# Performance work log

Measured on AMD Instinct MI355X. Metric: run time of the kernel, lower is better.

Reference implementation:

```python
import jax, jax.numpy as jnp
import numpy as np

BN_EPS = 1e-5

def setup_inputs() -> dict:
    key = jax.random.key(0)
    ks = jax.random.split(key, 12)
    B = 32768
    x = jax.random.normal(ks[0], (B, 1, 28, 28), dtype=jnp.float32)
    conv_w = jax.random.normal(ks[1], (5, 1, 6, 6), dtype=jnp.float32) * 0.1
    conv_b = jax.random.normal(ks[2], (5,), dtype=jnp.float32) * 0.1
    bn2_gamma = jnp.ones((5,), jnp.float32) + jax.random.normal(ks[3], (5,), jnp.float32) * 0.05
    bn2_beta = jax.random.normal(ks[4], (5,), jnp.float32) * 0.05
    bn2_mean = jax.random.normal(ks[5], (5,), jnp.float32) * 0.1
    bn2_var = jax.random.uniform(ks[6], (5,), jnp.float32, 0.5, 1.5)
    fc_w = jax.random.normal(ks[7], (10, 125), dtype=jnp.float32) * 0.1
    fc_b = jax.random.normal(ks[8], (10,), dtype=jnp.float32) * 0.1
    bn1_gamma = jnp.ones((10,), jnp.float32) + jax.random.normal(ks[9], (10,), jnp.float32) * 0.05
    bn1_beta = jax.random.normal(ks[10], (10,), jnp.float32) * 0.05
    bn1_mean = jax.random.normal(ks[11], (10,), jnp.float32) * 0.1
    bn1_var = jnp.ones((10,), jnp.float32)
    return {"x": x, "conv_w": conv_w, "conv_b": conv_b,
            "bn2_gamma": bn2_gamma, "bn2_beta": bn2_beta, "bn2_mean": bn2_mean, "bn2_var": bn2_var,
            "fc_w": fc_w, "fc_b": fc_b,
            "bn1_gamma": bn1_gamma, "bn1_beta": bn1_beta, "bn1_mean": bn1_mean, "bn1_var": bn1_var}

def _sign(t):
    # torch Binarize = tensor.sign()
    return jnp.sign(t)

def reference(x, conv_w, conv_b, bn2_gamma, bn2_beta, bn2_mean, bn2_var,
              fc_w, fc_b, bn1_gamma, bn1_beta, bn1_mean, bn1_var):
    # BinarizeConv2d: binarize both input (C_in=1 != 3) and weight
    xb = _sign(x)
    wb = _sign(conv_w)
    y = jax.lax.conv_general_dilated(
        xb, wb, window_strides=(6, 6), padding=((2, 2), (2, 2)),
        dimension_numbers=("NCHW", "OIHW", "NCHW"))  # [B,5,5,5]
    y = y + conv_b[None, :, None, None]
    # BatchNorm2d (eval-mode running stats)
    y = (y - bn2_mean[None, :, None, None]) * (bn2_gamma / jnp.sqrt(bn2_var + BN_EPS))[None, :, None, None] + bn2_beta[None, :, None, None]
    # Hardtanh
    y = jnp.clip(y, -1.0, 1.0)
    # flatten to [B, 125]
    y = y.reshape(-1, 125)
    # BinarizeLinear: binarize input (125 != 784) and weight
    z = _sign(y) @ _sign(fc_w).T + fc_b
    # BatchNorm1d
    z = (z - bn1_mean) * (bn1_gamma / jnp.sqrt(bn1_var + BN_EPS)) + bn1_beta
    return jax.nn.log_softmax(z, axis=1)
```

## Files before the change

### kernel.cpp

```cpp
#include <hip/hip_runtime.h>
#include <cstdint>

#define BLK 256
#define WAVES 4
#define SPW 4
#define SPB (WAVES*SPW)
#define WPS 196
#define HDRW 16
#define SLAB (SPW*WPS)
#define XS_INTS (HDRW + WAVES*SLAB)
#define YS_W 33
#define YSLAB (SPW*YS_W)

#define W0_OFF  0
#define W1P_OFF 30
#define FC_OFF  45
#define CSC_OFF 375
#define CBI_OFF 380
#define FSC_OFF 385
#define FBI_OFF 395
#define WS_TOT  405

#if defined(__has_builtin)
# if __has_builtin(__builtin_amdgcn_sdot4)
#  define HAVE_SDOT4 1
# endif
#endif

__device__ __forceinline__ int dot4i8(int a, int b, int c) {
#ifdef HAVE_SDOT4
    return __builtin_amdgcn_sdot4(a, b, c, false);
#else
    int r = c;
    r += (((int)(a << 24)) >> 24) * (((int)(b << 24)) >> 24);
    r += (((int)(a << 16)) >> 24) * (((int)(b << 16)) >> 24);
    r += (((int)(a <<  8)) >> 24) * (((int)(b <<  8)) >> 24);
    r += (a >> 24) * (b >> 24);
    return r;
#endif
}

__device__ __forceinline__ int pack_sign4(float4 v) {
    int b0 = (v.x > 0.f) - (v.x < 0.f);
    int b1 = (v.y > 0.f) - (v.y < 0.f);
    int b2 = (v.z > 0.f) - (v.z < 0.f);
    int b3 = (v.w > 0.f) - (v.w < 0.f);
    return (b0 & 0xFF) | ((b1 & 0xFF) << 8) | ((b2 & 0xFF) << 16) | (b3 << 24);
}

__device__ __forceinline__ int sign8(float f) { return (f > 0.f) - (f < 0.f); }

__global__ __launch_bounds__(BLK, 4)
void bnn_fused(const float* __restrict__ x,
               const float* __restrict__ conv_w, const float* __restrict__ conv_b,
               const float* __restrict__ bn2_g,  const float* __restrict__ bn2_b,
               const float* __restrict__ bn2_m,  const float* __restrict__ bn2_v,
               const float* __restrict__ fc_w,   const float* __restrict__ fc_b,
               const float* __restrict__ bn1_g,  const float* __restrict__ bn1_b,
               const float* __restrict__ bn1_m,  const float* __restrict__ bn1_v,
               float* __restrict__ out)
{
    __shared__ int xsi[XS_INTS];
    __shared__ int ysi[WAVES * YSLAB];
    __shared__ int wsS[WS_TOT];

    const int tid  = threadIdx.x;
    const int lane = tid & 63;
    const int wid  = tid >> 6;
    const int blk  = blockIdx.x;

    const float4* xg = (const float4*)x + ((size_t)blk * SPB + wid * SPW) * WPS;
    float4 v[12]; float4 vr;
    #pragma unroll
    for (int k = 0; k < 12; k++) v[k] = xg[lane + k * 64];
    const bool hasr = lane < (SLAB - 12 * 64);
    if (hasr) vr = xg[lane + 12 * 64];

    if (tid < 30) {
        int c = tid / 6, kr = tid - c * 6;
        const float* wp = conv_w + c * 36 + kr * 6;
        uint32_t a = 0;
        #pragma unroll
        for (int k = 0; k < 4; k++) a |= (uint32_t)(sign8(wp[k]) & 0xFF) << (8 * k);
        wsS[W0_OFF + tid] = (int)a;
    } else if (tid >= 32 && tid < 47) {
        int i = tid - 32, c = i / 3, p = i - c * 3;
        const float* wp = conv_w + c * 36;
        uint32_t a = 0;
        a |= (uint32_t)(sign8(wp[(2*p)*6 + 4]) & 0xFF);
        a |= (uint32_t)(sign8(wp[(2*p)*6 + 5]) & 0xFF) << 8;
        a |= (uint32_t)(sign8(wp[(2*p+1)*6 + 4]) & 0xFF) << 16;
        a |= (uint32_t)(sign8(wp[(2*p+1)*6 + 5]) & 0xFF) << 24;
        wsS[W1P_OFF + i] = (int)a;
    } else if (tid >= 48 && tid < 53) {
        int c = tid - 48;
        float sc = bn2_g[c] / sqrtf(bn2_v[c] + 1e-5f);
        wsS[CSC_OFF + c] = __float_as_int(sc);
        wsS[CBI_OFF + c] = __float_as_int((conv_b[c] - bn2_m[c]) * sc + bn2_b[c]);
    } else if (tid >= 64 && tid < 74) {
        int o = tid - 64;
        float sc = bn1_g[o] / sqrtf(bn1_v[o] + 1e-5f);
        wsS[FSC_OFF + o] = __float_as_int(sc);
        wsS[FBI_OFF + o] = __float_as_int((fc_b[o] - bn1_m[o]) * sc + bn1_b[o]);
    }
    for (int i = tid; i < 330; i += BLK) {
        int o = i / 33, w = i - o * 33;
        uint32_t m = 0;
        #pragma unroll
        for (int k = 0; k < 4; k++) {
            int kk = w * 4 + k;
            if (kk < 125) m |= (uint32_t)(sign8(fc_w[o * 125 + kk]) & 0xFF) << (8 * k);
        }
        wsS[FC_OFF + i] = (int)m;
    }
    if (tid < HDRW) xsi[tid] = 0;

    __syncthreads();

    ysi[wid * YSLAB + lane]      = 0;
    ysi[wid * YSLAB + lane + 64] = 0;
    if (lane < YSLAB - 128) ysi[wid * YSLAB + 128 + lane] = 0;

    int* xsw = xsi + HDRW + wid * SLAB;
    #pragma unroll
    for (int k = 0; k < 12; k++) xsw[lane + k * 64] = pack_sign4(v[k]);
    if (hasr) xsw[lane + 12 * 64] = pack_sign4(vr);

    {
        int w0[30], w1p[15]; float csc[5], cbi[5];
        #pragma unroll
        for (int i = 0; i < 30; i++) w0[i]  = wsS[W0_OFF + i];
        #pragma unroll
        for (int i = 0; i < 15; i++) w1p[i] = wsS[W1P_OFF + i];
        #pragma unroll
        for (int c = 0; c < 5; c++) {
            csc[c] = __int_as_float(wsS[CSC_OFF + c]);
            cbi[c] = __int_as_float(wsS[CBI_OFF + c]);
        }
        #pragma unroll
        for (int it = 0; it < 2; it++) {
            int jw = lane + it * 64;
            if (jw < SPW * 25) {
                int sl = jw / 25, pos = jw - sl * 25;
                int ss = wid * SPW + sl;
                int oh = pos / 5, ow  = pos - oh * 5;
                int rowb = ss * 784 + 168 * oh + 6 * ow - 58;
                int q  = (64 + rowb) >> 2;
                int sh = (rowb & 3) * 8;
                uint32_t emask = (ow == 0) ? 0xFFFF0000u : 0xFFFFFFFFu;
                uint32_t e0[6], e1[6];
                #pragma unroll
                for (int kr = 0; kr < 6; kr++) {
                    int a = q + 7 * kr;
                    if (kr < 2) a = (oh == 0) ? 0 : a;
                    uint32_t a0 = (uint32_t)xsi[a];
                    uint32_t a1 = (uint32_t)xsi[a + 1];
                    uint64_t vv = ((((uint64_t)a1) << 32) | a0) >> sh;
                    e0[kr] = (uint32_t)vv & emask;
                    e1[kr] = (uint32_t)(vv >> 32) & 0xFFFFu;
                }
                uint32_t e1p[3];
                #pragma unroll
                for (int p = 0; p < 3; p++) e1p[p] = e1[2*p] | (e1[2*p+1] << 16);
                #pragma unroll
                for (int c = 0; c < 5; c++) {
                    int acc = 0;
                    #pragma unroll
                    for (int kr = 0; kr < 6; kr++) acc = dot4i8((int)e0[kr], w0[c*6+kr], acc);
                    #pragma unroll
                    for (int p = 0; p < 3; p++)    acc = dot4i8((int)e1p[p], w1p[c*3+p], acc);
                    float yv = (float)acc * csc[c] + cbi[c];
                    ((signed char*)ysi)[(ss * YS_W) * 4 + c * 25 + pos] = (signed char)sign8(yv);
                }
            }
        }
    }

    {
        int sl = lane >> 4;
        int oo = lane & 15;
        int ss = wid * SPW + sl;
        int oc = (oo < 10) ? oo : 0;
        int acc = 0;
        #pragma unroll
        for (int w = 0; w < 32; w++)
            acc = dot4i8(ysi[ss * YS_W + w], wsS[FC_OFF + oc * 33 + w], acc);
        float z = (oo < 10)
            ? (float)acc * __int_as_float(wsS[FSC_OFF + oc]) + __int_as_float(wsS[FBI_OFF + oc])
            : -1e30f;
        float mx = z;
        #pragma unroll
        for (int m = 1; m < 16; m <<= 1) mx = fmaxf(mx, __shfl_xor(mx, m, 16));
        float e = (oo < 10) ? __expf(z - mx) : 0.f;
        float sum = e;
        #pragma unroll
        for (int m = 1; m < 16; m <<= 1) sum += __shfl_xor(sum, m, 16);
        float res = z - mx - __logf(sum);
        if (oo < 10)
            out[((size_t)blk * SPB + ss) * 10 + oo] = res;
    }
}

extern "C" void kernel_launch(void* const* d_in, const int* in_sizes, int n_in,
                              void* d_out, int out_size, void* d_ws, size_t ws_size,
                              hipStream_t stream)
{
    const float* xp     = (const float*)d_in[0];
    const float* conv_w = (const float*)d_in[1];
    const float* conv_b = (const float*)d_in[2];
    const float* bn2_g  = (const float*)d_in[3];
    const float* bn2_b  = (const float*)d_in[4];
    const float* bn2_m  = (const float*)d_in[5];
    const float* bn2_v  = (const float*)d_in[6];
    const float* fc_w   = (const float*)d_in[7];
    const float* fc_b   = (const float*)d_in[8];
    const float* bn1_g  = (const float*)d_in[9];
    const float* bn1_b  = (const float*)d_in[10];
    const float* bn1_m  = (const float*)d_in[11];
    const float* bn1_v  = (const float*)d_in[12];
    float* outp = (float*)d_out;

    const int B = in_sizes[0] / 784;
    const int grid = B / SPB;
    bnn_fused<<<grid, BLK, 0, stream>>>(xp, conv_w, conv_b,
                                        bn2_g, bn2_b, bn2_m, bn2_v,
                                        fc_w, fc_b, bn1_g, bn1_b, bn1_m, bn1_v,
                                        outp);
}
```

Measured before the change: 178.2 us.

## Loop each block over multiple sample tiles with register prefetch and double-buffered LDS

Each block now walks T=8 tiles of 8 samples instead of handling 16 samples once, so the weight-sign packing and BN-constant setup are paid once per block. While one tile is sign-packed and computed, the next tile's float4 inputs are loaded into registers, and the packed bits alternate between two LDS slabs. The grid shrinks fourfold and launch bounds drop to 2 blocks per SM, which cuts the number of waves resident and the loads in flight per CU. That lower memory-level parallelism could hurt this bandwidth-bound kernel.

Measured after the change: 180.3 us. About the same (+1.2%).

```diff
diff --git a/kernel.cpp b/kernel.cpp
--- a/kernel.cpp
+++ b/kernel.cpp
@@ -3,12 +3,12 @@
 
 #define BLK 256
 #define WAVES 4
-#define SPW 4
+#define SPW 2
 #define SPB (WAVES*SPW)
 #define WPS 196
 #define HDRW 16
-#define SLAB (SPW*WPS)
-#define XS_INTS (HDRW + WAVES*SLAB)
+#define SLABW (SPW*WPS)
+#define XS_INTS (HDRW + WAVES*2*SLABW)
 #define YS_W 33
 #define YSLAB (SPW*YS_W)
 
@@ -50,7 +50,7 @@
 
 __device__ __forceinline__ int sign8(float f) { return (f > 0.f) - (f < 0.f); }
 
-__global__ __launch_bounds__(BLK, 4)
+__global__ __launch_bounds__(BLK, 2)
 void bnn_fused(const float* __restrict__ x,
                const float* __restrict__ conv_w, const float* __restrict__ conv_b,
                const float* __restrict__ bn2_g,  const float* __restrict__ bn2_b,
@@ -58,7 +58,7 @@
                const float* __restrict__ fc_w,   const float* __restrict__ fc_b,
                const float* __restrict__ bn1_g,  const float* __restrict__ bn1_b,
                const float* __restrict__ bn1_m,  const float* __restrict__ bn1_v,
-               float* __restrict__ out)
+               float* __restrict__ out, int T)
 {
     __shared__ int xsi[XS_INTS];
     __shared__ int ysi[WAVES * YSLAB];
@@ -68,13 +68,6 @@
     const int lane = tid & 63;
     const int wid  = tid >> 6;
     const int blk  = blockIdx.x;
-
-    const float4* xg = (const float4*)x + ((size_t)blk * SPB + wid * SPW) * WPS;
-    float4 v[12]; float4 vr;
-    #pragma unroll
-    for (int k = 0; k < 12; k++) v[k] = xg[lane + k * 64];
-    const bool hasr = lane < (SLAB - 12 * 64);
-    if (hasr) vr = xg[lane + 12 * 64];
 
     if (tid < 30) {
         int c = tid / 6, kr = tid - c * 6;
@@ -117,87 +110,109 @@
 
     __syncthreads();
 
-    ysi[wid * YSLAB + lane]      = 0;
-    ysi[wid * YSLAB + lane + 64] = 0;
-    if (lane < YSLAB - 128) ysi[wid * YSLAB + 128 + lane] = 0;
-
-    int* xsw = xsi + HDRW + wid * SLAB;
+    int w0[30], w1p[15]; float csc[5], cbi[5];
     #pragma unroll
-    for (int k = 0; k < 12; k++) xsw[lane + k * 64] = pack_sign4(v[k]);
-    if (hasr) xsw[lane + 12 * 64] = pack_sign4(vr);
-
+    for (int i = 0; i < 30; i++) w0[i]  = wsS[W0_OFF + i];
+    #pragma unroll
+    for (int i = 0; i < 15; i++) w1p[i] = wsS[W1P_OFF + i];
+    #pragma unroll
+    for (int c = 0; c < 5; c++) {
+        csc[c] = __int_as_float(wsS[CSC_OFF + c]);
+        cbi[c] = __int_as_float(wsS[CBI_OFF + c]);
+    }
+    ysi[wid * YSLAB + lane] = 0;
+    if (lane < YSLAB - 64) ysi[wid * YSLAB + 64 + lane] = 0;
+
+    const float4* xb = (const float4*)x;
+    float4 v[6], vr, nv[6], nvr;
     {
-        int w0[30], w1p[15]; float csc[5], cbi[5];
-        #pragma unroll
-        for (int i = 0; i < 30; i++) w0[i]  = wsS[W0_OFF + i];
-        #pragma unroll
-        for (int i = 0; i < 15; i++) w1p[i] = wsS[W1P_OFF + i];
-        #pragma unroll
-        for (int c = 0; c < 5; c++) {
-            csc[c] = __int_as_float(wsS[CSC_OFF + c]);
-            cbi[c] = __int_as_float(wsS[CBI_OFF + c]);
-        }
-        #pragma unroll
-        for (int it = 0; it < 2; it++) {
-            int jw = lane + it * 64;
-            if (jw < SPW * 25) {
-                int sl = jw / 25, pos = jw - sl * 25;
-                int ss = wid * SPW + sl;
-                int oh = pos / 5, ow  = pos - oh * 5;
-                int rowb = ss * 784 + 168 * oh + 6 * ow - 58;
-                int q  = (64 + rowb) >> 2;
-                int sh = (rowb & 3) * 8;
-                uint32_t emask = (ow == 0) ? 0xFFFF0000u : 0xFFFFFFFFu;
-                uint32_t e0[6], e1[6];
-                #pragma unroll
-                for (int kr = 0; kr < 6; kr++) {
-                    int a = q + 7 * kr;
-                    if (kr < 2) a = (oh == 0) ? 0 : a;
-                    uint32_t a0 = (uint32_t)xsi[a];
-                    uint32_t a1 = (uint32_t)xsi[a + 1];
-                    uint64_t vv = ((((uint64_t)a1) << 32) | a0) >> sh;
-                    e0[kr] = (uint32_t)vv & emask;
-                    e1[kr] = (uint32_t)(vv >> 32) & 0xFFFFu;
-                }
-                uint32_t e1p[3];
-                #pragma unroll
-                for (int p = 0; p < 3; p++) e1p[p] = e1[2*p] | (e1[2*p+1] << 16);
-                #pragma unroll
-                for (int c = 0; c < 5; c++) {
-                    int acc = 0;
-                    #pragma unroll
-                    for (int kr = 0; kr < 6; kr++) acc = dot4i8((int)e0[kr], w0[c*6+kr], acc);
-                    #pragma unroll
-                    for (int p = 0; p < 3; p++)    acc = dot4i8((int)e1p[p], w1p[c*3+p], acc);
-                    float yv = (float)acc * csc[c] + cbi[c];
-                    ((signed char*)ysi)[(ss * YS_W) * 4 + c * 25 + pos] = (signed char)sign8(yv);
+        const float4* p = xb + (((size_t)blk * T) * SPB + wid * SPW) * WPS;
+        #pragma unroll
+        for (int k = 0; k < 6; k++) v[k] = p[lane + k * 64];
+        if (lane < SLABW - 384) vr = p[lane + 384];
+    }
+
+    for (int t = 0; t < T; ++t) {
+        if (t + 1 < T) {
+            const float4* p = xb + (((size_t)blk * T + (t + 1)) * SPB + wid * SPW) * WPS;
+            #pragma unroll
+            for (int k = 0; k < 6; k++) nv[k] = p[lane + k * 64];
+            if (lane < SLABW - 384) nvr = p[lane + 384];
+        }
+
+        const int slabW = HDRW + (wid * 2 + (t & 1)) * SLABW;
+        int* xsw = xsi + slabW;
+        #pragma unroll
+        for (int k = 0; k < 6; k++) xsw[lane + k * 64] = pack_sign4(v[k]);
+        if (lane < SLABW - 384) xsw[lane + 384] = pack_sign4(vr);
+
+        if (lane < SPW * 25) {
+            int sl  = lane >= 25;
+            int pos = lane - 25 * sl;
+            int oh = pos / 5, ow = pos - oh * 5;
+            int rowb = sl * 784 + 168 * oh + 6 * ow - 58;
+            int q  = (slabW * 4 + rowb) >> 2;
+            int sh = (rowb & 3) * 8;
+            uint32_t emask = (ow == 0) ? 0xFFFF0000u : 0xFFFFFFFFu;
+            uint32_t e0[6], e1[6];
+            #pragma unroll
+            for (int kr = 0; kr < 6; kr++) {
+                int a = q + 7 * kr;
+                if (kr < 2) a = (oh == 0) ? 0 : a;
+                uint32_t a0 = (uint32_t)xsi[a];
+                uint32_t a1 = (uint32_t)xsi[a + 1];
+                uint64_t vv = ((((uint64_t)a1) << 32) | a0) >> sh;
+                e0[kr] = (uint32_t)vv & emask;
+                e1[kr] = (uint32_t)(vv >> 32) & 0xFFFFu;
+            }
+            uint32_t e1p[3];
+            #pragma unroll
+            for (int p = 0; p < 3; p++) e1p[p] = e1[2*p] | (e1[2*p+1] << 16);
+            #pragma unroll
+            for (int c = 0; c < 5; c++) {
+                int acc = 0;
+                #pragma unroll
+                for (int kr = 0; kr < 6; kr++) acc = dot4i8((int)e0[kr], w0[c*6+kr], acc);
+                #pragma unroll
+                for (int p = 0; p < 3; p++)    acc = dot4i8((int)e1p[p], w1p[c*3+p], acc);
+                float yv = (float)acc * csc[c] + cbi[c];
+                ((signed char*)ysi)[(wid * YSLAB + sl * YS_W) * 4 + c * 25 + pos] =
+                    (signed char)sign8(yv);
+            }
+        }
+
+        {
+            int sl = (lane >> 4) & 1;
+            int oo = lane & 15;
+            int oc = (oo < 10) ? oo : 0;
+            if (lane < 32) {
+                int acc = 0;
+                #pragma unroll
+                for (int w = 0; w < 32; w++)
+                    acc = dot4i8(ysi[wid * YSLAB + sl * YS_W + w], wsS[FC_OFF + oc * 33 + w], acc);
+                float z = (oo < 10)
+                    ? (float)acc * __int_as_float(wsS[FSC_OFF + oc]) + __int_as_float(wsS[FBI_OFF + oc])
+                    : -1e30f;
+                float mx = z;
+                #pragma unroll
+                for (int m = 1; m < 16; m <<= 1) mx = fmaxf(mx, __shfl_xor(mx, m, 16));
+                float e = (oo < 10) ? __expf(z - mx) : 0.f;
+                float sum = e;
+                #pragma unroll
+                for (int m = 1; m < 16; m <<= 1) sum += __shfl_xor(sum, m, 16);
+                if (oo < 10) {
+                    float res = z - mx - __logf(sum);
+                    size_t si = ((size_t)blk * T + t) * SPB + wid * SPW + sl;
+                    out[si * 10 + oo] = res;
                 }
             }
         }
-    }
-
-    {
-        int sl = lane >> 4;
-        int oo = lane & 15;
-        int ss = wid * SPW + sl;
-        int oc = (oo < 10) ? oo : 0;
-        int acc = 0;
-        #pragma unroll
-        for (int w = 0; w < 32; w++)
-            acc = dot4i8(ysi[ss * YS_W + w], wsS[FC_OFF + oc * 33 + w], acc);
-        float z = (oo < 10)
-            ? (float)acc * __int_as_float(wsS[FSC_OFF + oc]) + __int_as_float(wsS[FBI_OFF + oc])
-            : -1e30f;
-        float mx = z;
-        #pragma unroll
-        for (int m = 1; m < 16; m <<= 1) mx = fmaxf(mx, __shfl_xor(mx, m, 16));
-        float e = (oo < 10) ? __expf(z - mx) : 0.f;
-        float sum = e;
-        #pragma unroll
-        for (int m = 1; m < 16; m <<= 1) sum += __shfl_xor(sum, m, 16);
-        float res = z - mx - __logf(sum);
-        if (oo < 10)
-            out[((size_t)blk * SPB + ss) * 10 + oo] = res;
+
+        if (t + 1 < T) {
+            #pragma unroll
+            for (int k = 0; k < 6; k++) v[k] = nv[k];
+            vr = nvr;
+        }
     }
 }
 
@@ -221,9 +236,10 @@
     float* outp = (float*)d_out;
 
     const int B = in_sizes[0] / 784;
-    const int grid = B / SPB;
+    const int T = 8;
+    const int grid = B / (SPB * T);
     bnn_fused<<<grid, BLK, 0, stream>>>(xp, conv_w, conv_b,
                                         bn2_g, bn2_b, bn2_m, bn2_v,
                                         fc_w, fc_b, bn1_g, bn1_b, bn1_m, bn1_v,
-                                        outp);
-}
+                                        outp, T);
+}
```
